# Optimization experiments

Measured on AMD Instinct MI355X. Metric: run time of the kernel, lower is better.

Reference implementation:

```python
import jax, jax.numpy as jnp
import numpy as np
import math

B, NQ, NK = 8, 1024, 2048
DQ = DK = DV = 1024
H = 8
DH = DV // H
EPS = 1e-5


def _layernorm(x, g, b):
    mu = jnp.mean(x, axis=-1, keepdims=True)
    var = jnp.mean(jnp.square(x - mu), axis=-1, keepdims=True)
    return (x - mu) * jax.lax.rsqrt(var + EPS) * g + b


def setup_inputs() -> dict:
    key = jax.random.key(0)
    ks = jax.random.split(key, 12)
    s_q = 1.0 / math.sqrt(DQ)
    s_v = 1.0 / math.sqrt(DV)
    return {
        "Q": jax.random.normal(ks[0], (B, NQ, DQ), jnp.float32),
        "K": jax.random.normal(ks[1], (B, NK, DK), jnp.float32),
        "Wq": jax.random.normal(ks[2], (DQ, DV), jnp.float32) * s_q,
        "bq": jnp.zeros((DV,), jnp.float32),
        "Wk": jax.random.normal(ks[3], (DK, DV), jnp.float32) * s_q,
        "bk": jnp.zeros((DV,), jnp.float32),
        "Wv": jax.random.normal(ks[4], (DK, DV), jnp.float32) * s_q,
        "bv": jnp.zeros((DV,), jnp.float32),
        "Wo": jax.random.normal(ks[5], (DV, DV), jnp.float32) * s_v,
        "bo": jnp.zeros((DV,), jnp.float32),
        "g0": jnp.ones((DV,), jnp.float32),
        "b0": jnp.zeros((DV,), jnp.float32),
        "g1": jnp.ones((DV,), jnp.float32),
        "b1": jnp.zeros((DV,), jnp.float32),
    }


def reference(Q, K, Wq, bq, Wk, bk, Wv, bv, Wo, bo, g0, b0, g1, b1):
    # projections
    q = Q @ Wq + bq                      # [B, NQ, DV]
    k = K @ Wk + bk                      # [B, NK, DV]
    v = K @ Wv + bv                      # [B, NK, DV]
    qh = q.reshape(B, NQ, H, DH)
    kh = k.reshape(B, NK, H, DH)
    vh = v.reshape(B, NK, H, DH)
    # NOTE: original scales by sqrt(dim_V), not sqrt(d_head)
    scale = 1.0 / math.sqrt(DV)
    logits = jnp.einsum("bqhd,bkhd->bhqk", qh, kh) * scale
    A = jax.nn.softmax(logits, axis=-1)
    # residual baked into attention output: Q_ + A @ V_
    Oh = qh + jnp.einsum("bhqk,bkhd->bqhd", A, vh)
    O = Oh.reshape(B, NQ, DV)
    O = _layernorm(O, g0, b0)
    O = O + jax.nn.relu(O @ Wo + bo)
    O = _layernorm(O, g1, b1)
    return O
```

## Files before the change

kernel.cpp:

```cpp
#include <hip/hip_runtime.h>
#include <stdint.h>

#define DEVI static __device__ __forceinline__

typedef __attribute__((ext_vector_type(8))) short short8;
typedef __attribute__((ext_vector_type(4))) float floatx4;
typedef __attribute__((ext_vector_type(4))) unsigned short ushortx4;

DEVI unsigned short f2bf(float f) {
  union { float f; uint32_t u; } v; v.f = f;
  uint32_t r = v.u + 0x7FFFu + ((v.u >> 16) & 1u);
  return (unsigned short)(r >> 16);
}
DEVI unsigned short f2bf_trunc(float f) {
  union { float f; uint32_t u; } v; v.f = f;
  return (unsigned short)(v.u >> 16);
}
DEVI float bf2f(unsigned short s) {
  union { uint32_t u; float f; } v; v.u = ((uint32_t)s) << 16;
  return v.f;
}
DEVI uint32_t fbits(float f) {
  union { float f; uint32_t u; } v; v.f = f;
  return v.u;
}
DEVI unsigned char f2fp8(float f) {
  return (unsigned char)(__builtin_amdgcn_cvt_pk_fp8_f32(f, f, 0, false) & 0xff);
}

DEVI void lds_cp16(void* lds, const void* g) {
  __builtin_amdgcn_global_load_lds(
      (const __attribute__((address_space(1))) uint32_t*)g,
      reinterpret_cast<__attribute__((address_space(3))) uint32_t*>(
          (uint32_t)reinterpret_cast<uintptr_t>(lds)),
      16, 0, 0);
}

__global__ __launch_bounds__(256) void cvt_qk(const float* __restrict__ Q,
                                              const float* __restrict__ K,
                                              unsigned short* __restrict__ Qb,
                                              unsigned char* __restrict__ Kf8) {
  const int bid = blockIdx.x;
  if (bid < 8192) {
    const size_t i = (size_t)bid * 256 + threadIdx.x;
    const floatx4 v = ((const floatx4*)Q)[i];
    ushortx4 o;
    o.x = f2bf(v.x); o.y = f2bf(v.y); o.z = f2bf(v.z); o.w = f2bf(v.w);
    ((ushortx4*)Qb)[i] = o;
  } else {
    const size_t i = (size_t)(bid - 8192) * 256 + threadIdx.x;
    const floatx4 v = ((const floatx4*)K)[i];
    int p = __builtin_amdgcn_cvt_pk_fp8_f32(v.x, v.y, 0, false);
    p = __builtin_amdgcn_cvt_pk_fp8_f32(v.z, v.w, p, true);
    ((int*)Kf8)[i] = p;
  }
}

__global__ __launch_bounds__(256) void wtrans4(const float* __restrict__ Wq,
                                               const float* __restrict__ Wk,
                                               const float* __restrict__ Wv,
                                               const float* __restrict__ Wo,
                                               unsigned short* __restrict__ Wt,
                                               unsigned char* __restrict__ Wt8) {
  __shared__ float t[32][33];
  const int tx = threadIdx.x, ty = threadIdx.y;
  const int z = blockIdx.z;
  const float* W = (z == 0) ? Wq : (z == 1) ? Wk : (z == 2) ? Wv : Wo;
  const int c0 = blockIdx.x * 32, r0 = blockIdx.y * 32;
#pragma unroll
  for (int i = 0; i < 4; i++)
    t[ty + i * 8][tx] = W[(size_t)(r0 + ty + i * 8) * 1024 + c0 + tx];
  __syncthreads();
  if (z == 0 || z == 3) {
    unsigned short* D = Wt + (z == 0 ? 0 : (size_t)1024 * 1024);
#pragma unroll
    for (int i = 0; i < 4; i++)
      D[(size_t)(c0 + ty + i * 8) * 1024 + r0 + tx] = f2bf(t[tx][ty + i * 8]);
  } else {
    unsigned char* D = Wt8 + (z == 1 ? 0 : (size_t)1024 * 1024);
#pragma unroll
    for (int i = 0; i < 4; i++)
      D[(size_t)(c0 + ty + i * 8) * 1024 + r0 + tx] = f2fp8(t[tx][ty + i * 8]);
  }
}

template <int EPI>
__global__ __launch_bounds__(256, 3) void gemm_bt(
    const unsigned short* __restrict__ A, const unsigned short* __restrict__ Bt,
    const float* __restrict__ bias, const unsigned short* __restrict__ X1,
    void* __restrict__ Cout) {
  __shared__ unsigned short As[2][4][128][8];
  __shared__ unsigned short Bs[2][4][128][8];

  const int tid = threadIdx.x;
  const int lane = tid & 63, w = tid >> 6;
  const int wr = w >> 1, wc = w & 1;
  const int qd = lane >> 4, l16 = lane & 15;
  const int bid = blockIdx.x;
  const int xcd = bid & 7, loc = bid >> 3;
  const int m0 = (xcd * 8 + (loc & 7)) * 128;
  const int n0 = (loc >> 3) * 128;

  floatx4 acc[4][4];
#pragma unroll
  for (int i = 0; i < 4; i++)
#pragma unroll
    for (int j = 0; j < 4; j++) { floatx4 z = {0.f, 0.f, 0.f, 0.f}; acc[i][j] = z; }

  const int prow = tid & 127;
  const unsigned short* aptr = A + (size_t)(m0 + prow) * 1024 + ((tid >> 7) << 3);
  const unsigned short* bptr = Bt + (size_t)(n0 + prow) * 1024 + ((tid >> 7) << 3);
  const int dstoff = tid * 8;

  lds_cp16(&As[0][0][0][0] + dstoff, aptr);
  lds_cp16(&As[0][0][0][0] + dstoff + 2048, aptr + 16);
  lds_cp16(&Bs[0][0][0][0] + dstoff, bptr);
  lds_cp16(&Bs[0][0][0][0] + dstoff + 2048, bptr + 16);

  for (int it = 0; it < 32; it++) {
    __syncthreads();
    if (it < 31) {
      const int nb = (it + 1) & 1, k0 = (it + 1) * 32;
      lds_cp16(&As[nb][0][0][0] + dstoff, aptr + k0);
      lds_cp16(&As[nb][0][0][0] + dstoff + 2048, aptr + k0 + 16);
      lds_cp16(&Bs[nb][0][0][0] + dstoff, bptr + k0);
      lds_cp16(&Bs[nb][0][0][0] + dstoff + 2048, bptr + k0 + 16);
    }
    const int cur = it & 1;
    short8 af[4], bf[4];
#pragma unroll
    for (int mi = 0; mi < 4; mi++)
      af[mi] = *(const short8*)&As[cur][qd][wr * 64 + mi * 16 + l16][0];
#pragma unroll
    for (int ni = 0; ni < 4; ni++)
      bf[ni] = *(const short8*)&Bs[cur][qd][wc * 64 + ni * 16 + l16][0];
#pragma unroll
    for (int mi = 0; mi < 4; mi++)
#pragma unroll
      for (int ni = 0; ni < 4; ni++)
        acc[mi][ni] =
            __builtin_amdgcn_mfma_f32_16x16x32_bf16(af[mi], bf[ni], acc[mi][ni], 0, 0, 0);
  }

#pragma unroll
  for (int mi = 0; mi < 4; mi++) {
#pragma unroll
    for (int ni = 0; ni < 4; ni++) {
      const int row = m0 + wr * 64 + mi * 16 + qd * 4;
      const int col = n0 + wc * 64 + ni * 16 + l16;
      const float bv = bias[col];
      if constexpr (EPI == 0) {
        unsigned short* C = (unsigned short*)Cout;
#pragma unroll
        for (int r = 0; r < 4; r++)
          C[(size_t)(row + r) * 1024 + col] = f2bf(acc[mi][ni][r] + bv);
      } else {
        float* C = (float*)Cout;
#pragma unroll
        for (int r = 0; r < 4; r++) {
          const float x1 = bf2f(X1[(size_t)(row + r) * 1024 + col]);
          C[(size_t)(row + r) * 1024 + col] = x1 + fmaxf(acc[mi][ni][r] + bv, 0.f);
        }
      }
    }
  }
}

__global__ __launch_bounds__(256, 3) void gemm_kv_f8(
    const unsigned char* __restrict__ A, const unsigned char* __restrict__ Bt,
    const float* __restrict__ biasK, const float* __restrict__ biasV,
    unsigned short* __restrict__ CK, unsigned short* __restrict__ CV) {
  __shared__ unsigned char As[2][4][128][16];
  __shared__ unsigned char Bs[2][4][128][16];

  const int tid = threadIdx.x;
  const int lane = tid & 63, w = tid >> 6;
  const int wr = w >> 1, wc = w & 1;
  const int qd = lane >> 4, l16 = lane & 15;
  const int bid = blockIdx.x;
  const int xcd = bid & 7, loc = bid >> 3;
  const int m0 = (xcd * 16 + (loc & 15)) * 128;
  const int n0 = (loc >> 4) * 128;

  floatx4 acc[4][4];
#pragma unroll
  for (int i = 0; i < 4; i++)
#pragma unroll
    for (int j = 0; j < 4; j++) { floatx4 z = {0.f, 0.f, 0.f, 0.f}; acc[i][j] = z; }

  const int srow = tid & 127, sc = tid >> 7;
  const unsigned char* aptr = A + (size_t)(m0 + srow) * 1024 + sc * 16;
  const unsigned char* bptr = Bt + (size_t)(n0 + srow) * 1024 + sc * 16;
  unsigned char* dA = &As[0][sc][srow][0];
  unsigned char* dB = &Bs[0][sc][srow][0];

  lds_cp16(dA, aptr);
  lds_cp16(dA + 4096, aptr + 32);
  lds_cp16(dB, bptr);
  lds_cp16(dB + 4096, bptr + 32);

  for (int it = 0; it < 16; it++) {
    __syncthreads();
    if (it < 15) {
      const int nb = (it + 1) & 1, k0 = (it + 1) * 64;
      lds_cp16(dA + nb * 8192, aptr + k0);
      lds_cp16(dA + nb * 8192 + 4096, aptr + k0 + 32);
      lds_cp16(dB + nb * 8192, bptr + k0);
      lds_cp16(dB + nb * 8192 + 4096, bptr + k0 + 32);
    }
    const int cur = it & 1;
    const int coff = (qd & 1) * 8, chi = qd >> 1;
    long a8[4][2], b8[4][2];
#pragma unroll
    for (int mi = 0; mi < 4; mi++) {
      const int row = wr * 64 + mi * 16 + l16;
      a8[mi][0] = *(const long*)&As[cur][chi][row][coff];
      a8[mi][1] = *(const long*)&As[cur][2 + chi][row][coff];
    }
#pragma unroll
    for (int ni = 0; ni < 4; ni++) {
      const int row = wc * 64 + ni * 16 + l16;
      b8[ni][0] = *(const long*)&Bs[cur][chi][row][coff];
      b8[ni][1] = *(const long*)&Bs[cur][2 + chi][row][coff];
    }
#pragma unroll
    for (int mi = 0; mi < 4; mi++)
#pragma unroll
      for (int ni = 0; ni < 4; ni++)
        acc[mi][ni] = __builtin_amdgcn_mfma_f32_16x16x32_fp8_fp8(
            a8[mi][0], b8[ni][0], acc[mi][ni], 0, 0, 0);
#pragma unroll
    for (int mi = 0; mi < 4; mi++)
#pragma unroll
      for (int ni = 0; ni < 4; ni++)
        acc[mi][ni] = __builtin_amdgcn_mfma_f32_16x16x32_fp8_fp8(
            a8[mi][1], b8[ni][1], acc[mi][ni], 0, 0, 0);
  }

#pragma unroll
  for (int mi = 0; mi < 4; mi++) {
#pragma unroll
    for (int ni = 0; ni < 4; ni++) {
      const int row = m0 + wr * 64 + mi * 16 + qd * 4;
      const int col = n0 + wc * 64 + ni * 16 + l16;
      if (col < 1024) {
        const float bv = biasK[col];
#pragma unroll
        for (int r = 0; r < 4; r++)
          CK[(size_t)(row + r) * 1024 + col] = f2bf(acc[mi][ni][r] + bv);
      } else {
        const int vc = col - 1024;
        const float bv = biasV[vc];
        const int bb = row >> 11, nk = row & 2047;
        const int hh = vc >> 7, dh = vc & 127;
        ushortx4 pk;
        pk.x = f2bf(acc[mi][ni][0] + bv);
        pk.y = f2bf(acc[mi][ni][1] + bv);
        pk.z = f2bf(acc[mi][ni][2] + bv);
        pk.w = f2bf(acc[mi][ni][3] + bv);
        *(ushortx4*)&CV[(size_t)((bb * 8 + hh) * 128 + dh) * 2048 + nk] = pk;
      }
    }
  }
}

__global__ __launch_bounds__(256, 3) void attn(
    const unsigned short* __restrict__ qb, const unsigned short* __restrict__ kb,
    const unsigned short* __restrict__ vt, unsigned short* __restrict__ Ob) {
  __shared__ unsigned short smem[16384];

  const int tid = threadIdx.x;
  const int lane = tid & 63, w = tid >> 6;
  const int qd = lane >> 4, l16 = lane & 15;
  const int bid = blockIdx.x;
  const int qt = bid >> 6, bh = bid & 63;
  const int h = bh >> 3, b = bh & 7;
  const int m0 = qt * 128;

  const size_t qbase = ((size_t)(b * 1024 + m0)) * 1024 + h * 128;
  const size_t kbase = ((size_t)(b * 2048)) * 1024 + h * 128;
  const size_t vbase = ((size_t)((b * 8 + h) * 128)) * 2048;

#pragma unroll
  for (int i = 0; i < 8; i++) {
    const int p = i * 256 + tid;
    const int row = p & 127, c = p >> 7;
    lds_cp16(&smem[c * 1024 + row * 8], qb + qbase + (size_t)row * 1024 + c * 8);
  }
  __syncthreads();
  short8 qf[2][4];
#pragma unroll
  for (int nt = 0; nt < 2; nt++)
#pragma unroll
    for (int ks = 0; ks < 4; ks++)
      qf[nt][ks] =
          *(const short8*)&smem[(ks * 4 + qd) * 1024 + (w * 32 + nt * 16 + l16) * 8];
  __syncthreads();

#pragma unroll
  for (int i = 0; i < 2; i++) {
    const int p = i * 256 + tid;
    const int kr = p & 31, kc = p >> 5;
    lds_cp16(&smem[kc * 256 + kr * 8], kb + kbase + (size_t)kr * 1024 + kc * 8);
    const int dh = p & 127, vc = p >> 7;
    lds_cp16(&smem[8192 + vc * 1024 + dh * 8], vt + vbase + (size_t)dh * 2048 + vc * 8);
  }

  floatx4 oacc[8][2];
#pragma unroll
  for (int mt = 0; mt < 8; mt++)
#pragma unroll
    for (int nt = 0; nt < 2; nt++) { floatx4 z = {0.f, 0.f, 0.f, 0.f}; oacc[mt][nt] = z; }
  float lsum[2] = {0.f, 0.f};

  const int addrLo = ((qd & 1) * 32 + l16) * 4;
  const int addrHi = addrLo + 64;
  const bool loHalf = (lane < 32);

  for (int it = 0; it < 64; it++) {
    __syncthreads();
    if (it + 1 < 64) {
      const int nb = (it + 1) & 1, kv0 = (it + 1) * 32;
#pragma unroll
      for (int i = 0; i < 2; i++) {
        const int p = i * 256 + tid;
        const int kr = p & 31, kc = p >> 5;
        lds_cp16(&smem[nb * 4096 + kc * 256 + kr * 8],
                 kb + kbase + (size_t)(kv0 + kr) * 1024 + kc * 8);
        const int dh = p & 127, vc = p >> 7;
        lds_cp16(&smem[8192 + nb * 4096 + vc * 1024 + dh * 8],
                 vt + vbase + (size_t)dh * 2048 + kv0 + vc * 8);
      }
    }
    const int cur = it & 1;

    floatx4 st[2][2];
#pragma unroll
    for (int mt = 0; mt < 2; mt++)
#pragma unroll
      for (int nt = 0; nt < 2; nt++) { floatx4 z = {0.f, 0.f, 0.f, 0.f}; st[mt][nt] = z; }
#pragma unroll
    for (int ks = 0; ks < 4; ks++) {
      const short8 ka = *(const short8*)&smem[cur * 4096 + (ks * 4 + qd) * 256 + l16 * 8];
      const short8 kb2 =
          *(const short8*)&smem[cur * 4096 + (ks * 4 + qd) * 256 + (16 + l16) * 8];
#pragma unroll
      for (int nt = 0; nt < 2; nt++) {
        st[0][nt] = __builtin_amdgcn_mfma_f32_16x16x32_bf16(ka, qf[nt][ks], st[0][nt], 0, 0, 0);
        st[1][nt] = __builtin_amdgcn_mfma_f32_16x16x32_bf16(kb2, qf[nt][ks], st[1][nt], 0, 0, 0);
      }
    }

    uint32_t pk[2][2][2];
#pragma unroll
    for (int mt = 0; mt < 2; mt++)
#pragma unroll
      for (int nt = 0; nt < 2; nt++) {
        const float e0 = __expf(st[mt][nt][0] * 0.03125f);
        const float e1 = __expf(st[mt][nt][1] * 0.03125f);
        const float e2 = __expf(st[mt][nt][2] * 0.03125f);
        const float e3 = __expf(st[mt][nt][3] * 0.03125f);
        lsum[nt] += (e0 + e1) + (e2 + e3);
        pk[mt][nt][0] = __builtin_amdgcn_perm(fbits(e1), fbits(e0), 0x07060302);
        pk[mt][nt][1] = __builtin_amdgcn_perm(fbits(e3), fbits(e2), 0x07060302);
      }

#pragma unroll
    for (int nt = 0; nt < 2; nt++) {
      int d0a = __builtin_amdgcn_ds_bpermute(addrLo, (int)pk[0][nt][0]);
      int d0b = __builtin_amdgcn_ds_bpermute(addrLo, (int)pk[1][nt][0]);
      int d1a = __builtin_amdgcn_ds_bpermute(addrLo, (int)pk[0][nt][1]);
      int d1b = __builtin_amdgcn_ds_bpermute(addrLo, (int)pk[1][nt][1]);
      int d2a = __builtin_amdgcn_ds_bpermute(addrHi, (int)pk[0][nt][0]);
      int d2b = __builtin_amdgcn_ds_bpermute(addrHi, (int)pk[1][nt][0]);
      int d3a = __builtin_amdgcn_ds_bpermute(addrHi, (int)pk[0][nt][1]);
      int d3b = __builtin_amdgcn_ds_bpermute(addrHi, (int)pk[1][nt][1]);
      union { int i[4]; short8 s; } u;
      u.i[0] = loHalf ? d0a : d0b;
      u.i[1] = loHalf ? d1a : d1b;
      u.i[2] = loHalf ? d2a : d2b;
      u.i[3] = loHalf ? d3a : d3b;
      const short8 pf = u.s;
#pragma unroll
      for (int mt = 0; mt < 8; mt++) {
        const short8 vf =
            *(const short8*)&smem[8192 + cur * 4096 + qd * 1024 + (mt * 16 + l16) * 8];
        oacc[mt][nt] = __builtin_amdgcn_mfma_f32_16x16x32_bf16(vf, pf, oacc[mt][nt], 0, 0, 0);
      }
    }
  }

  float inv[2];
#pragma unroll
  for (int nt = 0; nt < 2; nt++) {
    float s = lsum[nt];
    s += __shfl_xor(s, 16);
    s += __shfl_xor(s, 32);
    inv[nt] = 1.f / s;
  }

  __syncthreads();
#pragma unroll
  for (int mt = 0; mt < 8; mt++)
#pragma unroll
    for (int nt = 0; nt < 2; nt++) {
      const int q = w * 32 + nt * 16 + l16;
#pragma unroll
      for (int r = 0; r < 4; r++) {
        const int dh = mt * 16 + qd * 4 + r;
        const int c = dh >> 3, off = dh & 7;
        smem[q * 128 + ((c ^ (q & 15)) * 8) + off] = f2bf_trunc(oacc[mt][nt][r] * inv[nt]);
      }
    }
  __syncthreads();
#pragma unroll
  for (int i = 0; i < 8; i++) {
    const int p = i * 256 + tid;
    const int row = p >> 4, c = p & 15;
    const short8 ov = *(const short8*)&smem[row * 128 + ((c ^ (row & 15)) * 8)];
    const short8 qres = *(const short8*)(qb + qbase + (size_t)row * 1024 + c * 8);
    union { unsigned short us[8]; short8 s; } o;
#pragma unroll
    for (int e = 0; e < 8; e++)
      o.us[e] = f2bf(bf2f((unsigned short)ov[e]) + bf2f((unsigned short)qres[e]));
    *(short8*)(Ob + qbase + (size_t)row * 1024 + c * 8) = o.s;
  }
}

__global__ __launch_bounds__(256) void ln_rows(const unsigned short* __restrict__ X,
                                               const float* __restrict__ g,
                                               const float* __restrict__ bb,
                                               unsigned short* __restrict__ Y) {
  __shared__ float red[8];
  const int row = blockIdx.x, tid = threadIdx.x;
  const int w = tid >> 6, lane = tid & 63;
  const ushortx4 u = ((const ushortx4*)(X + (size_t)row * 1024))[tid];
  float x0 = bf2f(u.x), x1 = bf2f(u.y), x2 = bf2f(u.z), x3 = bf2f(u.w);
  float s = x0 + x1 + x2 + x3;
  float s2 = x0 * x0 + x1 * x1 + x2 * x2 + x3 * x3;
#pragma unroll
  for (int off = 1; off < 64; off <<= 1) { s += __shfl_xor(s, off); s2 += __shfl_xor(s2, off); }
  if (lane == 0) { red[w] = s; red[4 + w] = s2; }
  __syncthreads();
  s = red[0] + red[1] + red[2] + red[3];
  s2 = red[4] + red[5] + red[6] + red[7];
  const float mu = s * (1.f / 1024.f);
  const float rs = rsqrtf(s2 * (1.f / 1024.f) - mu * mu + 1e-5f);
  const floatx4 gv = ((const floatx4*)g)[tid];
  const floatx4 bv = ((const floatx4*)bb)[tid];
  ushortx4 o;
  o.x = f2bf((x0 - mu) * rs * gv.x + bv.x);
  o.y = f2bf((x1 - mu) * rs * gv.y + bv.y);
  o.z = f2bf((x2 - mu) * rs * gv.z + bv.z);
  o.w = f2bf((x3 - mu) * rs * gv.w + bv.w);
  ((ushortx4*)(Y + (size_t)row * 1024))[tid] = o;
}

__global__ __launch_bounds__(256) void ln_f32(const float* __restrict__ X,
                                              const float* __restrict__ g,
                                              const float* __restrict__ bb,
                                              float* __restrict__ out) {
  __shared__ float red[8];
  const int row = blockIdx.x, tid = threadIdx.x;
  const int w = tid >> 6, lane = tid & 63;
  const floatx4 xv = ((const floatx4*)(X + (size_t)row * 1024))[tid];
  float x0 = xv.x, x1 = xv.y, x2 = xv.z, x3 = xv.w;
  float s = x0 + x1 + x2 + x3;
  float s2 = x0 * x0 + x1 * x1 + x2 * x2 + x3 * x3;
#pragma unroll
  for (int off = 1; off < 64; off <<= 1) { s += __shfl_xor(s, off); s2 += __shfl_xor(s2, off); }
  if (lane == 0) { red[w] = s; red[4 + w] = s2; }
  __syncthreads();
  s = red[0] + red[1] + red[2] + red[3];
  s2 = red[4] + red[5] + red[6] + red[7];
  const float mu = s * (1.f / 1024.f);
  const float rs = rsqrtf(s2 * (1.f / 1024.f) - mu * mu + 1e-5f);
  const floatx4 gv = ((const floatx4*)g)[tid];
  const floatx4 bv = ((const floatx4*)bb)[tid];
  floatx4 o;
  o.x = (x0 - mu) * rs * gv.x + bv.x;
  o.y = (x1 - mu) * rs * gv.y + bv.y;
  o.z = (x2 - mu) * rs * gv.z + bv.z;
  o.w = (x3 - mu) * rs * gv.w + bv.w;
  ((floatx4*)(out + (size_t)row * 1024))[tid] = o;
}

extern "C" void kernel_launch(void* const* d_in, const int* in_sizes, int n_in,
                              void* d_out, int out_size, void* d_ws, size_t ws_size,
                              hipStream_t stream) {
  (void)in_sizes; (void)n_in; (void)out_size; (void)ws_size;
  const float* Q  = (const float*)d_in[0];
  const float* K  = (const float*)d_in[1];
  const float* Wq = (const float*)d_in[2];
  const float* bq = (const float*)d_in[3];
  const float* Wk = (const float*)d_in[4];
  const float* bk = (const float*)d_in[5];
  const float* Wv = (const float*)d_in[6];
  const float* bv = (const float*)d_in[7];
  const float* Wo = (const float*)d_in[8];
  const float* bo = (const float*)d_in[9];
  const float* g0 = (const float*)d_in[10];
  const float* b0 = (const float*)d_in[11];
  const float* g1 = (const float*)d_in[12];
  const float* b1 = (const float*)d_in[13];
  float* out = (float*)d_out;

  char* ws = (char*)d_ws;
  const size_t MB = 1u << 20;
  unsigned short* Qb  = (unsigned short*)(ws + 0);
  unsigned short* X1  = (unsigned short*)(ws + 16 * MB);
  unsigned short* Wt  = (unsigned short*)(ws + 32 * MB);
  unsigned char*  Wt8 = (unsigned char*)(ws + 36 * MB);
  unsigned char*  Kf8 = (unsigned char*)(ws + 38 * MB);
  unsigned short* qbp = (unsigned short*)(ws + 54 * MB);
  unsigned short* kbp = (unsigned short*)(ws + 70 * MB);
  unsigned short* vtp = (unsigned short*)(ws + 102 * MB);
  unsigned short* O   = Qb;
  float* O2 = (float*)(ws + 70 * MB);

  unsigned short* Wqt = Wt;
  unsigned short* Wot = Wt + (size_t)1024 * 1024;

  cvt_qk<<<24576, 256, 0, stream>>>(Q, K, Qb, Kf8);
  wtrans4<<<dim3(32, 32, 4), dim3(32, 8), 0, stream>>>(Wq, Wk, Wv, Wo, Wt, Wt8);

  gemm_bt<0><<<512, 256, 0, stream>>>(Qb, Wqt, bq, nullptr, qbp);
  gemm_kv_f8<<<2048, 256, 0, stream>>>(Kf8, Wt8, bk, bv, kbp, vtp);
  attn<<<512, 256, 0, stream>>>(qbp, kbp, vtp, O);
  ln_rows<<<8192, 256, 0, stream>>>(O, g0, b0, X1);
  gemm_bt<2><<<512, 256, 0, stream>>>(X1, Wot, bo, X1, O2);
  ln_f32<<<8192, 256, 0, stream>>>(O2, g1, b1, out);
}
```

Measured before the change: 430.9 us.

## Triple-buffer LDS loads with explicit vmcnt waits in GEMMs and attention

Switches the bf16 GEMM, fp8 KV GEMM and attention kernels from double to triple LDS buffering. Tiles are prefetched two iterations ahead, and __syncthreads is replaced by an explicit s_waitcnt on vmcnt plus a raw barrier, so only the oldest outstanding loads must finish before compute. The aim is to hide more global-to-LDS latency behind MFMA work. In exchange, LDS use per block grows by half, which may reduce occupancy, and correctness now depends on the hand-coded waitcnt encodings.

```diff
diff --git a/kernel.cpp b/kernel.cpp
--- a/kernel.cpp
+++ b/kernel.cpp
@@ -35,6 +35,10 @@
           (uint32_t)reinterpret_cast<uintptr_t>(lds)),
       16, 0, 0);
 }
+
+#define WAIT_VM4() __builtin_amdgcn_s_waitcnt(0x3F74)
+#define WAIT_VM0() __builtin_amdgcn_s_waitcnt(0x3F70)
+#define BAR() __builtin_amdgcn_s_barrier()
 
 __global__ __launch_bounds__(256) void cvt_qk(const float* __restrict__ Q,
                                               const float* __restrict__ K,
@@ -89,8 +93,8 @@
     const unsigned short* __restrict__ A, const unsigned short* __restrict__ Bt,
     const float* __restrict__ bias, const unsigned short* __restrict__ X1,
     void* __restrict__ Cout) {
-  __shared__ unsigned short As[2][4][128][8];
-  __shared__ unsigned short Bs[2][4][128][8];
+  __shared__ unsigned short As[3 * 4096];
+  __shared__ unsigned short Bs[3 * 4096];
 
   const int tid = threadIdx.x;
   const int lane = tid & 63, w = tid >> 6;
@@ -112,34 +116,41 @@
   const unsigned short* bptr = Bt + (size_t)(n0 + prow) * 1024 + ((tid >> 7) << 3);
   const int dstoff = tid * 8;
 
-  lds_cp16(&As[0][0][0][0] + dstoff, aptr);
-  lds_cp16(&As[0][0][0][0] + dstoff + 2048, aptr + 16);
-  lds_cp16(&Bs[0][0][0][0] + dstoff, bptr);
-  lds_cp16(&Bs[0][0][0][0] + dstoff + 2048, bptr + 16);
-
+#pragma unroll
+  for (int pb = 0; pb < 2; pb++) {
+    const int k0 = pb * 32;
+    lds_cp16(&As[pb * 4096] + dstoff, aptr + k0);
+    lds_cp16(&As[pb * 4096] + dstoff + 2048, aptr + k0 + 16);
+    lds_cp16(&Bs[pb * 4096] + dstoff, bptr + k0);
+    lds_cp16(&Bs[pb * 4096] + dstoff + 2048, bptr + k0 + 16);
+  }
+
+  int cur = 0;
   for (int it = 0; it < 32; it++) {
-    __syncthreads();
-    if (it < 31) {
-      const int nb = (it + 1) & 1, k0 = (it + 1) * 32;
-      lds_cp16(&As[nb][0][0][0] + dstoff, aptr + k0);
-      lds_cp16(&As[nb][0][0][0] + dstoff + 2048, aptr + k0 + 16);
-      lds_cp16(&Bs[nb][0][0][0] + dstoff, bptr + k0);
-      lds_cp16(&Bs[nb][0][0][0] + dstoff + 2048, bptr + k0 + 16);
-    }
-    const int cur = it & 1;
+    if (it < 31) WAIT_VM4(); else WAIT_VM0();
+    BAR();
+    if (it + 2 < 32) {
+      const int nb3 = cur == 0 ? 2 : cur - 1;
+      const int k0 = (it + 2) * 32;
+      lds_cp16(&As[nb3 * 4096] + dstoff, aptr + k0);
+      lds_cp16(&As[nb3 * 4096] + dstoff + 2048, aptr + k0 + 16);
+      lds_cp16(&Bs[nb3 * 4096] + dstoff, bptr + k0);
+      lds_cp16(&Bs[nb3 * 4096] + dstoff + 2048, bptr + k0 + 16);
+    }
     short8 af[4], bf[4];
 #pragma unroll
     for (int mi = 0; mi < 4; mi++)
-      af[mi] = *(const short8*)&As[cur][qd][wr * 64 + mi * 16 + l16][0];
+      af[mi] = *(const short8*)&As[cur * 4096 + qd * 1024 + (wr * 64 + mi * 16 + l16) * 8];
 #pragma unroll
     for (int ni = 0; ni < 4; ni++)
-      bf[ni] = *(const short8*)&Bs[cur][qd][wc * 64 + ni * 16 + l16][0];
+      bf[ni] = *(const short8*)&Bs[cur * 4096 + qd * 1024 + (wc * 64 + ni * 16 + l16) * 8];
 #pragma unroll
     for (int mi = 0; mi < 4; mi++)
 #pragma unroll
       for (int ni = 0; ni < 4; ni++)
         acc[mi][ni] =
             __builtin_amdgcn_mfma_f32_16x16x32_bf16(af[mi], bf[ni], acc[mi][ni], 0, 0, 0);
+    cur = cur == 2 ? 0 : cur + 1;
   }
 
 #pragma unroll
@@ -170,8 +181,8 @@
     const unsigned char* __restrict__ A, const unsigned char* __restrict__ Bt,
     const float* __restrict__ biasK, const float* __restrict__ biasV,
     unsigned short* __restrict__ CK, unsigned short* __restrict__ CV) {
-  __shared__ unsigned char As[2][4][128][16];
-  __shared__ unsigned char Bs[2][4][128][16];
+  __shared__ unsigned char As[3 * 8192];
+  __shared__ unsigned char Bs[3 * 8192];
 
   const int tid = threadIdx.x;
   const int lane = tid & 63, w = tid >> 6;
@@ -191,37 +202,42 @@
   const int srow = tid & 127, sc = tid >> 7;
   const unsigned char* aptr = A + (size_t)(m0 + srow) * 1024 + sc * 16;
   const unsigned char* bptr = Bt + (size_t)(n0 + srow) * 1024 + sc * 16;
-  unsigned char* dA = &As[0][sc][srow][0];
-  unsigned char* dB = &Bs[0][sc][srow][0];
-
-  lds_cp16(dA, aptr);
-  lds_cp16(dA + 4096, aptr + 32);
-  lds_cp16(dB, bptr);
-  lds_cp16(dB + 4096, bptr + 32);
-
+  const int doff = sc * 2048 + srow * 16;
+
+#pragma unroll
+  for (int pb = 0; pb < 2; pb++) {
+    const int k0 = pb * 64;
+    lds_cp16(&As[pb * 8192 + doff], aptr + k0);
+    lds_cp16(&As[pb * 8192 + doff + 4096], aptr + k0 + 32);
+    lds_cp16(&Bs[pb * 8192 + doff], bptr + k0);
+    lds_cp16(&Bs[pb * 8192 + doff + 4096], bptr + k0 + 32);
+  }
+
+  int cur = 0;
   for (int it = 0; it < 16; it++) {
-    __syncthreads();
-    if (it < 15) {
-      const int nb = (it + 1) & 1, k0 = (it + 1) * 64;
-      lds_cp16(dA + nb * 8192, aptr + k0);
-      lds_cp16(dA + nb * 8192 + 4096, aptr + k0 + 32);
-      lds_cp16(dB + nb * 8192, bptr + k0);
-      lds_cp16(dB + nb * 8192 + 4096, bptr + k0 + 32);
-    }
-    const int cur = it & 1;
+    if (it < 15) WAIT_VM4(); else WAIT_VM0();
+    BAR();
+    if (it + 2 < 16) {
+      const int nb3 = cur == 0 ? 2 : cur - 1;
+      const int k0 = (it + 2) * 64;
+      lds_cp16(&As[nb3 * 8192 + doff], aptr + k0);
+      lds_cp16(&As[nb3 * 8192 + doff + 4096], aptr + k0 + 32);
+      lds_cp16(&Bs[nb3 * 8192 + doff], bptr + k0);
+      lds_cp16(&Bs[nb3 * 8192 + doff + 4096], bptr + k0 + 32);
+    }
     const int coff = (qd & 1) * 8, chi = qd >> 1;
     long a8[4][2], b8[4][2];
 #pragma unroll
     for (int mi = 0; mi < 4; mi++) {
       const int row = wr * 64 + mi * 16 + l16;
-      a8[mi][0] = *(const long*)&As[cur][chi][row][coff];
-      a8[mi][1] = *(const long*)&As[cur][2 + chi][row][coff];
+      a8[mi][0] = *(const long*)&As[cur * 8192 + chi * 2048 + row * 16 + coff];
+      a8[mi][1] = *(const long*)&As[cur * 8192 + (2 + chi) * 2048 + row * 16 + coff];
     }
 #pragma unroll
     for (int ni = 0; ni < 4; ni++) {
       const int row = wc * 64 + ni * 16 + l16;
-      b8[ni][0] = *(const long*)&Bs[cur][chi][row][coff];
-      b8[ni][1] = *(const long*)&Bs[cur][2 + chi][row][coff];
+      b8[ni][0] = *(const long*)&Bs[cur * 8192 + chi * 2048 + row * 16 + coff];
+      b8[ni][1] = *(const long*)&Bs[cur * 8192 + (2 + chi) * 2048 + row * 16 + coff];
     }
 #pragma unroll
     for (int mi = 0; mi < 4; mi++)
@@ -235,6 +251,7 @@
       for (int ni = 0; ni < 4; ni++)
         acc[mi][ni] = __builtin_amdgcn_mfma_f32_16x16x32_fp8_fp8(
             a8[mi][1], b8[ni][1], acc[mi][ni], 0, 0, 0);
+    cur = cur == 2 ? 0 : cur + 1;
   }
 
 #pragma unroll
@@ -267,7 +284,7 @@
 __global__ __launch_bounds__(256, 3) void attn(
     const unsigned short* __restrict__ qb, const unsigned short* __restrict__ kb,
     const unsigned short* __restrict__ vt, unsigned short* __restrict__ Ob) {
-  __shared__ unsigned short smem[16384];
+  __shared__ unsigned short smem[24576];
 
   const int tid = threadIdx.x;
   const int lane = tid & 63, w = tid >> 6;
@@ -297,13 +314,20 @@
           *(const short8*)&smem[(ks * 4 + qd) * 1024 + (w * 32 + nt * 16 + l16) * 8];
   __syncthreads();
 
-#pragma unroll
-  for (int i = 0; i < 2; i++) {
-    const int p = i * 256 + tid;
-    const int kr = p & 31, kc = p >> 5;
-    lds_cp16(&smem[kc * 256 + kr * 8], kb + kbase + (size_t)kr * 1024 + kc * 8);
-    const int dh = p & 127, vc = p >> 7;
-    lds_cp16(&smem[8192 + vc * 1024 + dh * 8], vt + vbase + (size_t)dh * 2048 + vc * 8);
+  const int p0 = tid, p1 = 256 + tid;
+  const int kr0 = p0 & 31, kc0 = p0 >> 5, kr1 = p1 & 31, kc1 = p1 >> 5;
+  const int dh0 = p0 & 127, vc0 = p0 >> 7, dh1 = p1 & 127, vc1 = p1 >> 7;
+#pragma unroll
+  for (int pb = 0; pb < 2; pb++) {
+    const int kv0 = pb * 32;
+    lds_cp16(&smem[pb * 4096 + kc0 * 256 + kr0 * 8],
+             kb + kbase + (size_t)(kv0 + kr0) * 1024 + kc0 * 8);
+    lds_cp16(&smem[12288 + pb * 4096 + vc0 * 1024 + dh0 * 8],
+             vt + vbase + (size_t)dh0 * 2048 + kv0 + vc0 * 8);
+    lds_cp16(&smem[pb * 4096 + kc1 * 256 + kr1 * 8],
+             kb + kbase + (size_t)(kv0 + kr1) * 1024 + kc1 * 8);
+    lds_cp16(&smem[12288 + pb * 4096 + vc1 * 1024 + dh1 * 8],
+             vt + vbase + (size_t)dh1 * 2048 + kv0 + vc1 * 8);
   }
 
   floatx4 oacc[8][2];
@@ -317,22 +341,22 @@
   const int addrHi = addrLo + 64;
   const bool loHalf = (lane < 32);
 
+  int cur = 0;
   for (int it = 0; it < 64; it++) {
-    __syncthreads();
-    if (it + 1 < 64) {
-      const int nb = (it + 1) & 1, kv0 = (it + 1) * 32;
-#pragma unroll
-      for (int i = 0; i < 2; i++) {
-        const int p = i * 256 + tid;
-        const int kr = p & 31, kc = p >> 5;
-        lds_cp16(&smem[nb * 4096 + kc * 256 + kr * 8],
-                 kb + kbase + (size_t)(kv0 + kr) * 1024 + kc * 8);
-        const int dh = p & 127, vc = p >> 7;
-        lds_cp16(&smem[8192 + nb * 4096 + vc * 1024 + dh * 8],
-                 vt + vbase + (size_t)dh * 2048 + kv0 + vc * 8);
-      }
-    }
-    const int cur = it & 1;
+    if (it < 63) WAIT_VM4(); else WAIT_VM0();
+    BAR();
+    if (it + 2 < 64) {
+      const int nb3 = cur == 0 ? 2 : cur - 1;
+      const int kv0 = (it + 2) * 32;
+      lds_cp16(&smem[nb3 * 4096 + kc0 * 256 + kr0 * 8],
+               kb + kbase + (size_t)(kv0 + kr0) * 1024 + kc0 * 8);
+      lds_cp16(&smem[12288 + nb3 * 4096 + vc0 * 1024 + dh0 * 8],
+               vt + vbase + (size_t)dh0 * 2048 + kv0 + vc0 * 8);
+      lds_cp16(&smem[nb3 * 4096 + kc1 * 256 + kr1 * 8],
+               kb + kbase + (size_t)(kv0 + kr1) * 1024 + kc1 * 8);
+      lds_cp16(&smem[12288 + nb3 * 4096 + vc1 * 1024 + dh1 * 8],
+               vt + vbase + (size_t)dh1 * 2048 + kv0 + vc1 * 8);
+    }
 
     floatx4 st[2][2];
 #pragma unroll
@@ -384,10 +408,11 @@
 #pragma unroll
       for (int mt = 0; mt < 8; mt++) {
         const short8 vf =
-            *(const short8*)&smem[8192 + cur * 4096 + qd * 1024 + (mt * 16 + l16) * 8];
+            *(const short8*)&smem[12288 + cur * 4096 + qd * 1024 + (mt * 16 + l16) * 8];
         oacc[mt][nt] = __builtin_amdgcn_mfma_f32_16x16x32_bf16(vf, pf, oacc[mt][nt], 0, 0, 0);
       }
     }
+    cur = cur == 2 ? 0 : cur + 1;
   }
 
   float inv[2];
```

Result: slower. 443.5 us (+2.9%).
